# Optimization experiments

Hardware: AMD Instinct MI355X
Metric: run time of the kernel (lower is better)

Reference implementation:

```python
import jax, jax.numpy as jnp
import numpy as np

N_NODES = 40000
N_EDGES = 640000
D = 128
NEG_SLOPE = 0.2
EPS = 0.0  # init_eps=0, learn_eps=False -> constant buffer


def setup_inputs() -> dict:
    key = jax.random.key(0)
    ks = jax.random.split(key, 9)
    return {
        "feat": jax.random.normal(ks[0], (N_NODES, D), dtype=jnp.float32),
        "W_src": jax.random.normal(ks[1], (D, D), dtype=jnp.float32) * 0.1,
        "W_dst": jax.random.normal(ks[2], (D, D), dtype=jnp.float32) * 0.1,
        "W_src2": jax.random.normal(ks[3], (D, D), dtype=jnp.float32) * 0.1,
        "W_dst2": jax.random.normal(ks[4], (D, D), dtype=jnp.float32) * 0.1,
        "attn_l": jax.random.normal(ks[5], (D,), dtype=jnp.float32) * 0.1,
        "attn_r": jax.random.normal(ks[6], (D,), dtype=jnp.float32) * 0.1,
        "src": jax.random.randint(ks[7], (N_EDGES,), 0, N_NODES, dtype=jnp.int32),
        "dst": jax.random.randint(ks[8], (N_EDGES,), 0, N_NODES, dtype=jnp.int32),
    }


def reference(feat, W_src, W_dst, W_src2, W_dst2, attn_l, attn_r, src, dst):
    n = feat.shape[0]
    # Four linear projections (no bias), nn.Linear applies x @ W.T
    fs1 = feat @ W_src.T    # [N, D] -> messages for GIN sum
    fd1 = feat @ W_dst.T    # [N, D] -> self term
    fs2 = feat @ W_src2.T   # [N, D] -> attention-weighted messages
    fd2 = feat @ W_dst2.T   # [N, D]

    # GAT-style per-node attention logits
    el = jnp.sum(fs2 * attn_l, axis=-1)  # [N]
    er = jnp.sum(fd2 * attn_r, axis=-1)  # [N]

    # Per-edge score: u_add_v + leaky_relu
    e = el[src] + er[dst]                                   # [E]
    e = jnp.where(e >= 0, e, NEG_SLOPE * e)

    # edge_softmax: segment-wise softmax over edges grouped by dst
    seg_max = jax.ops.segment_max(e, dst, num_segments=n)   # [N]
    seg_max = jnp.where(jnp.isfinite(seg_max), seg_max, 0.0)
    ex = jnp.exp(e - seg_max[dst])                          # [E]
    denom = jax.ops.segment_sum(ex, dst, num_segments=n)    # [N]
    a = ex / denom[dst]                                     # [E]

    # update_all(copy_u, sum): plain neighbor sum of fs1
    neigh = jax.ops.segment_sum(fs1[src], dst, num_segments=n)            # [N, D]
    # update_all(u_mul_e, sum): attention-weighted sum of fs2
    add_ft = jax.ops.segment_sum(fs2[src] * a[:, None], dst, num_segments=n)  # [N, D]

    rst = (1.0 + EPS) * fd1 + neigh + add_ft
    return rst
```

## Files before the change

kernel.cpp:

```cpp
#include <hip/hip_runtime.h>
#include <math.h>

#define N_NODES 40000
#define N_EDGES 640000
#define D 128
#define NEG_SLOPE 0.2f
#define BCAP 64

typedef __bf16 bf16x8 __attribute__((ext_vector_type(8)));
typedef float f32x4 __attribute__((ext_vector_type(4)));

__device__ __forceinline__ unsigned short f2bf(float f) {
    unsigned int u = __float_as_uint(f);
    return (unsigned short)((u + 0x7fffu + ((u >> 16) & 1u)) >> 16);
}
__device__ __forceinline__ float bflo(unsigned int u) { return __uint_as_float(u << 16); }
__device__ __forceinline__ float bfhi(unsigned int u) { return __uint_as_float(u & 0xffff0000u); }

__global__ void k_zero_v(uint4* __restrict__ cnt4,
                         const float* __restrict__ Ws2, const float* __restrict__ Wd2,
                         const float* __restrict__ attn_l, const float* __restrict__ attn_r,
                         float* __restrict__ v_l, float* __restrict__ v_r) {
    if (blockIdx.x == 40) {
        int t = threadIdx.x;
        if (t < 128) {
            float s = 0.0f;
            for (int j = 0; j < D; ++j) s += attn_l[j] * Ws2[j * D + t];
            v_l[t] = s;
        } else {
            int k = t - 128;
            float s = 0.0f;
            for (int j = 0; j < D; ++j) s += attn_r[j] * Wd2[j * D + k];
            v_r[k] = s;
        }
        return;
    }
    int i = blockIdx.x * 256 + threadIdx.x;
    if (i < 10000) cnt4[i] = make_uint4(0, 0, 0, 0);
}

__global__ void k_setup(const float* __restrict__ Ws, const float* __restrict__ Ws2,
                        const float* __restrict__ Wd,
                        unsigned short* __restrict__ Wfrag,
                        const float* __restrict__ v_l, const float* __restrict__ v_r,
                        const int* __restrict__ src, const int* __restrict__ dst,
                        int* __restrict__ cnt, unsigned short* __restrict__ bucket,
                        const float* __restrict__ feat, unsigned int* __restrict__ featb,
                        float* __restrict__ el, float* __restrict__ er) {
    if (blockIdx.x < 625) {
        int t = blockIdx.x * 256 + threadIdx.x;
        #pragma unroll
        for (int j = 0; j < 4; ++j) {
            int e = t + j * 160000;
            int d = dst[e];
            int s = src[e];
            int slot = atomicAdd(&cnt[d], 1);
            if (slot < BCAP) bucket[(size_t)d * BCAP + slot] = (unsigned short)s;
        }
        return;
    }
    if (blockIdx.x < 817) {
        int idx = (blockIdx.x - 625) * 256 + threadIdx.x;
        int e    = idx & 7;
        int lane = (idx >> 3) & 63;
        int ks   = (idx >> 9) & 3;
        int ct   = (idx >> 11) & 7;
        int m    = idx >> 14;
        int col  = ct * 16 + (lane & 15);
        int k    = ks * 32 + (lane >> 4) * 8 + e;
        const float* W = (m == 0) ? Ws : (m == 1) ? Ws2 : Wd;
        Wfrag[idx] = f2bf(W[col * D + k]);
        return;
    }
    int idx = blockIdx.x - 817;
    int row = idx * 16 + (threadIdx.x >> 4);
    int c   = threadIdx.x & 15;
    const float* fp = feat + (size_t)row * D + c * 8;
    float4 p = *(const float4*)fp;
    float4 q = *(const float4*)(fp + 4);
    uint4 u;
    u.x = (unsigned int)f2bf(p.x) | ((unsigned int)f2bf(p.y) << 16);
    u.y = (unsigned int)f2bf(p.z) | ((unsigned int)f2bf(p.w) << 16);
    u.z = (unsigned int)f2bf(q.x) | ((unsigned int)f2bf(q.y) << 16);
    u.w = (unsigned int)f2bf(q.z) | ((unsigned int)f2bf(q.w) << 16);
    *(uint4*)(featb + (size_t)row * 64 + c * 4) = u;
    const float* vlp = v_l + c * 8;
    const float* vrp = v_r + c * 8;
    float4 l0 = *(const float4*)vlp, l1 = *(const float4*)(vlp + 4);
    float4 r0 = *(const float4*)vrp, r1 = *(const float4*)(vrp + 4);
    float sl = p.x*l0.x + p.y*l0.y + p.z*l0.z + p.w*l0.w
             + q.x*l1.x + q.y*l1.y + q.z*l1.z + q.w*l1.w;
    float sr = p.x*r0.x + p.y*r0.y + p.z*r0.z + p.w*r0.w
             + q.x*r1.x + q.y*r1.y + q.z*r1.z + q.w*r1.w;
    #pragma unroll
    for (int w = 1; w <= 8; w <<= 1) {
        sl += __shfl_xor(sl, w);
        sr += __shfl_xor(sr, w);
    }
    if (c == 0) { el[row] = sl; er[row] = sr; }
}

__global__ __launch_bounds__(256) void k_aggregate(
    const int* __restrict__ cnt, const unsigned short* __restrict__ bucket,
    const float* __restrict__ el, const float* __restrict__ er,
    const unsigned int* __restrict__ featb,
    unsigned int* __restrict__ agg1b, unsigned int* __restrict__ agg2b)
{
    const int node = blockIdx.x * 4 + (threadIdx.x >> 6);
    const int lane = threadIdx.x & 63;
    if (node >= N_NODES) return;
    int deg = cnt[node];
    deg = (deg > BCAP) ? BCAP : deg;

    const int q = lane & 15;
    const int g = lane >> 4;
    float A1[8], A2[8];
    #pragma unroll
    for (int c = 0; c < 8; ++c) { A1[c] = 0.f; A2[c] = 0.f; }

    if (deg > 0) {
        const int base = node * BCAP;
        int s_l = bucket[base + lane];
        if (lane >= deg) s_l = 0;

        uint4 v[8];
        #pragma unroll
        for (int j = 0; j < 8; ++j) {
            int eidx = (j >> 2) * 16 + (j & 3) * 4 + g;
            int s = __shfl(s_l, eidx);
            v[j] = *(const uint4*)(featb + (size_t)s * 64 + q * 4);
        }

        const float ern = er[node];
        float e = -INFINITY;
        if (lane < deg) {
            e = el[s_l] + ern;
            e = (e >= 0.f) ? e : NEG_SLOPE * e;
        }
        float mx = e;
        #pragma unroll
        for (int w = 32; w >= 1; w >>= 1) mx = fmaxf(mx, __shfl_xor(mx, w));
        float p = (lane < deg) ? __expf(e - mx) : 0.f;
        float ssum = p;
        #pragma unroll
        for (int w = 32; w >= 1; w >>= 1) ssum += __shfl_xor(ssum, w);
        float a_l = p / ssum;

        #pragma unroll
        for (int j = 0; j < 4; ++j) {
            int eidx = (j & 3) * 4 + g;
            float av = __shfl(a_l, eidx);
            float wf = (eidx < deg) ? 1.0f : 0.0f;
            float x0 = bflo(v[j].x), x1 = bfhi(v[j].x);
            float x2 = bflo(v[j].y), x3 = bfhi(v[j].y);
            float x4 = bflo(v[j].z), x5 = bfhi(v[j].z);
            float x6 = bflo(v[j].w), x7 = bfhi(v[j].w);
            A1[0] += wf * x0; A2[0] += av * x0;
            A1[1] += wf * x1; A2[1] += av * x1;
            A1[2] += wf * x2; A2[2] += av * x2;
            A1[3] += wf * x3; A2[3] += av * x3;
            A1[4] += wf * x4; A2[4] += av * x4;
            A1[5] += wf * x5; A2[5] += av * x5;
            A1[6] += wf * x6; A2[6] += av * x6;
            A1[7] += wf * x7; A2[7] += av * x7;
        }
        if (deg > 16) {
            #pragma unroll
            for (int j = 4; j < 8; ++j) {
                int eidx = 16 + (j & 3) * 4 + g;
                float av = __shfl(a_l, eidx);
                float wf = (eidx < deg) ? 1.0f : 0.0f;
                float x0 = bflo(v[j].x), x1 = bfhi(v[j].x);
                float x2 = bflo(v[j].y), x3 = bfhi(v[j].y);
                float x4 = bflo(v[j].z), x5 = bfhi(v[j].z);
                float x6 = bflo(v[j].w), x7 = bfhi(v[j].w);
                A1[0] += wf * x0; A2[0] += av * x0;
                A1[1] += wf * x1; A2[1] += av * x1;
                A1[2] += wf * x2; A2[2] += av * x2;
                A1[3] += wf * x3; A2[3] += av * x3;
                A1[4] += wf * x4; A2[4] += av * x4;
                A1[5] += wf * x5; A2[5] += av * x5;
                A1[6] += wf * x6; A2[6] += av * x6;
                A1[7] += wf * x7; A2[7] += av * x7;
            }
            for (int i = 32; i < deg; i += 16) {
                uint4 vt[4];
                float av[4], wf[4];
                #pragma unroll
                for (int j = 0; j < 4; ++j) {
                    int eidx = i + j * 4 + g;
                    int s = __shfl(s_l, eidx);
                    av[j] = __shfl(a_l, eidx);
                    wf[j] = (eidx < deg) ? 1.0f : 0.0f;
                    vt[j] = *(const uint4*)(featb + (size_t)s * 64 + q * 4);
                }
                #pragma unroll
                for (int j = 0; j < 4; ++j) {
                    float x0 = bflo(vt[j].x), x1 = bfhi(vt[j].x);
                    float x2 = bflo(vt[j].y), x3 = bfhi(vt[j].y);
                    float x4 = bflo(vt[j].z), x5 = bfhi(vt[j].z);
                    float x6 = bflo(vt[j].w), x7 = bfhi(vt[j].w);
                    A1[0] += wf[j] * x0; A2[0] += av[j] * x0;
                    A1[1] += wf[j] * x1; A2[1] += av[j] * x1;
                    A1[2] += wf[j] * x2; A2[2] += av[j] * x2;
                    A1[3] += wf[j] * x3; A2[3] += av[j] * x3;
                    A1[4] += wf[j] * x4; A2[4] += av[j] * x4;
                    A1[5] += wf[j] * x5; A2[5] += av[j] * x5;
                    A1[6] += wf[j] * x6; A2[6] += av[j] * x6;
                    A1[7] += wf[j] * x7; A2[7] += av[j] * x7;
                }
            }
        }

        #pragma unroll
        for (int c = 0; c < 8; ++c) {
            A1[c] += __shfl_xor(A1[c], 16); A1[c] += __shfl_xor(A1[c], 32);
            A2[c] += __shfl_xor(A2[c], 16); A2[c] += __shfl_xor(A2[c], 32);
        }
    }

    if (lane < 16) {
        uint4 u1, u2;
        u1.x = (unsigned int)f2bf(A1[0]) | ((unsigned int)f2bf(A1[1]) << 16);
        u1.y = (unsigned int)f2bf(A1[2]) | ((unsigned int)f2bf(A1[3]) << 16);
        u1.z = (unsigned int)f2bf(A1[4]) | ((unsigned int)f2bf(A1[5]) << 16);
        u1.w = (unsigned int)f2bf(A1[6]) | ((unsigned int)f2bf(A1[7]) << 16);
        u2.x = (unsigned int)f2bf(A2[0]) | ((unsigned int)f2bf(A2[1]) << 16);
        u2.y = (unsigned int)f2bf(A2[2]) | ((unsigned int)f2bf(A2[3]) << 16);
        u2.z = (unsigned int)f2bf(A2[4]) | ((unsigned int)f2bf(A2[5]) << 16);
        u2.w = (unsigned int)f2bf(A2[6]) | ((unsigned int)f2bf(A2[7]) << 16);
        *(uint4*)(agg1b + (size_t)node * 64 + q * 4) = u1;
        *(uint4*)(agg2b + (size_t)node * 64 + q * 4) = u2;
    }
}

__global__ __launch_bounds__(256) void k_gemm_all(
    const unsigned int* __restrict__ featb,
    const unsigned int* __restrict__ agg1b, const unsigned int* __restrict__ agg2b,
    const unsigned short* __restrict__ Wfrag, float* __restrict__ out)
{
    const int lane = threadIdx.x & 63;
    const int wave = threadIdx.x >> 6;
    const int tile = blockIdx.x >> 1;
    const int cth  = (blockIdx.x & 1) * 4;
    const int row0 = tile * 64 + wave * 16;
    const int arow = row0 + (lane & 15);
    const int koff = (lane >> 4) * 4;

    bf16x8 af[4], a1[4], a2[4];
    #pragma unroll
    for (int ks = 0; ks < 4; ++ks) {
        size_t o = (size_t)arow * 64 + ks * 16 + koff;
        af[ks] = *(const bf16x8*)(featb + o);
        a1[ks] = *(const bf16x8*)(agg1b + o);
        a2[ks] = *(const bf16x8*)(agg2b + o);
    }

    const bf16x8* wf0 = (const bf16x8*)Wfrag;
    const bf16x8* wf1 = wf0 + (size_t)(8 * 4) * 64;
    const bf16x8* wf2 = wf0 + (size_t)(2 * 8 * 4) * 64;

    f32x4 acc[4];
    #pragma unroll
    for (int c = 0; c < 4; ++c) acc[c] = (f32x4){0.f, 0.f, 0.f, 0.f};
    #pragma unroll
    for (int ks = 0; ks < 4; ++ks) {
        #pragma unroll
        for (int c = 0; c < 4; ++c) {
            const size_t bo = (size_t)((cth + c) * 4 + ks) * 64 + lane;
            acc[c] = __builtin_amdgcn_mfma_f32_16x16x32_bf16(af[ks], wf2[bo], acc[c], 0, 0, 0);
            acc[c] = __builtin_amdgcn_mfma_f32_16x16x32_bf16(a1[ks], wf0[bo], acc[c], 0, 0, 0);
            acc[c] = __builtin_amdgcn_mfma_f32_16x16x32_bf16(a2[ks], wf1[bo], acc[c], 0, 0, 0);
        }
    }

    const int rbase = row0 + (lane >> 4) * 4;
    const int cbase = lane & 15;
    #pragma unroll
    for (int c = 0; c < 4; ++c)
        #pragma unroll
        for (int r = 0; r < 4; ++r)
            out[(size_t)(rbase + r) * D + (cth + c) * 16 + cbase] = acc[c][r];
}

extern "C" void kernel_launch(void* const* d_in, const int* in_sizes, int n_in,
                              void* d_out, int out_size, void* d_ws, size_t ws_size,
                              hipStream_t stream) {
    const float* feat   = (const float*)d_in[0];
    const float* W_src  = (const float*)d_in[1];
    const float* W_dst  = (const float*)d_in[2];
    const float* W_src2 = (const float*)d_in[3];
    const float* W_dst2 = (const float*)d_in[4];
    const float* attn_l = (const float*)d_in[5];
    const float* attn_r = (const float*)d_in[6];
    const int*   src    = (const int*)d_in[7];
    const int*   dst    = (const int*)d_in[8];
    float* out = (float*)d_out;

    char* w = (char*)d_ws;
    float* v_l = (float*)w;                       w += 128 * 4;
    float* v_r = (float*)w;                       w += 128 * 4;
    float* el  = (float*)w;                       w += N_NODES * 4;
    float* er  = (float*)w;                       w += N_NODES * 4;
    int* cnt   = (int*)w;                         w += N_NODES * 4;
    unsigned int* featb = (unsigned int*)w;       w += (size_t)N_NODES * 64 * 4;
    unsigned int* agg1b = (unsigned int*)w;       w += (size_t)N_NODES * 64 * 4;
    unsigned int* agg2b = (unsigned int*)w;       w += (size_t)N_NODES * 64 * 4;
    unsigned short* bucket = (unsigned short*)w;  w += (size_t)N_NODES * BCAP * 2;
    unsigned short* Wfrag = (unsigned short*)w;   w += 3 * 8 * 4 * 64 * 8 * 2;

    k_zero_v<<<41, 256, 0, stream>>>((uint4*)cnt, W_src2, W_dst2, attn_l, attn_r, v_l, v_r);

    k_setup<<<3317, 256, 0, stream>>>(W_src, W_src2, W_dst, Wfrag, v_l, v_r,
                                      src, dst, cnt, bucket, feat, featb, el, er);

    k_aggregate<<<(N_NODES + 3) / 4, 256, 0, stream>>>(cnt, bucket, el, er,
                                                       featb, agg1b, agg2b);

    k_gemm_all<<<1250, 256, 0, stream>>>(featb, agg1b, agg2b, Wfrag, out);
}
```

Before: 98.73 us.

## Replace per-node global atomics with two-phase binned bucketing via shared-memory counters

```diff
diff --git a/kernel.cpp b/kernel.cpp
--- a/kernel.cpp
+++ b/kernel.cpp
@@ -6,6 +6,8 @@
 #define D 128
 #define NEG_SLOPE 0.2f
 #define BCAP 64
+#define NBINS 1250
+#define BINCAP 1024
 
 typedef __bf16 bf16x8 __attribute__((ext_vector_type(8)));
 typedef float f32x4 __attribute__((ext_vector_type(4)));
@@ -17,11 +19,11 @@
 __device__ __forceinline__ float bflo(unsigned int u) { return __uint_as_float(u << 16); }
 __device__ __forceinline__ float bfhi(unsigned int u) { return __uint_as_float(u & 0xffff0000u); }
 
-__global__ void k_zero_v(uint4* __restrict__ cnt4,
+__global__ void k_zero_v(int* __restrict__ binCnt,
                          const float* __restrict__ Ws2, const float* __restrict__ Wd2,
                          const float* __restrict__ attn_l, const float* __restrict__ attn_r,
                          float* __restrict__ v_l, float* __restrict__ v_r) {
-    if (blockIdx.x == 40) {
+    if (blockIdx.x == 5) {
         int t = threadIdx.x;
         if (t < 128) {
             float s = 0.0f;
@@ -36,7 +38,7 @@
         return;
     }
     int i = blockIdx.x * 256 + threadIdx.x;
-    if (i < 10000) cnt4[i] = make_uint4(0, 0, 0, 0);
+    if (i < NBINS) binCnt[i] = 0;
 }
 
 __global__ void k_setup(const float* __restrict__ Ws, const float* __restrict__ Ws2,
@@ -44,7 +46,7 @@
                         unsigned short* __restrict__ Wfrag,
                         const float* __restrict__ v_l, const float* __restrict__ v_r,
                         const int* __restrict__ src, const int* __restrict__ dst,
-                        int* __restrict__ cnt, unsigned short* __restrict__ bucket,
+                        int* __restrict__ binCnt, unsigned int* __restrict__ binBuf,
                         const float* __restrict__ feat, unsigned int* __restrict__ featb,
                         float* __restrict__ el, float* __restrict__ er) {
     if (blockIdx.x < 625) {
@@ -54,8 +56,11 @@
             int e = t + j * 160000;
             int d = dst[e];
             int s = src[e];
-            int slot = atomicAdd(&cnt[d], 1);
-            if (slot < BCAP) bucket[(size_t)d * BCAP + slot] = (unsigned short)s;
+            int b = d >> 5;
+            int dlow = d & 31;
+            int slot = atomicAdd(&binCnt[b], 1);
+            if (slot < BINCAP)
+                binBuf[(size_t)b * BINCAP + slot] = (unsigned int)s | ((unsigned int)dlow << 16);
         }
         return;
     }
@@ -100,6 +105,31 @@
     if (c == 0) { el[row] = sl; er[row] = sr; }
 }
 
+__global__ __launch_bounds__(256) void k_phaseB(
+    const int* __restrict__ binCnt, const unsigned int* __restrict__ binBuf,
+    unsigned short* __restrict__ bucket, int* __restrict__ cnt)
+{
+    __shared__ int lcnt[32];
+    const int b = blockIdx.x;
+    if (threadIdx.x < 32) lcnt[threadIdx.x] = 0;
+    __syncthreads();
+    int n = binCnt[b];
+    n = (n > BINCAP) ? BINCAP : n;
+    for (int i = threadIdx.x; i < n; i += 256) {
+        unsigned int ent = binBuf[(size_t)b * BINCAP + i];
+        int s    = ent & 0xffff;
+        int dlow = ent >> 16;
+        int slot = atomicAdd(&lcnt[dlow], 1);
+        if (slot < BCAP)
+            bucket[(size_t)(b * 32 + dlow) * BCAP + slot] = (unsigned short)s;
+    }
+    __syncthreads();
+    if (threadIdx.x < 32) {
+        int v = lcnt[threadIdx.x];
+        cnt[b * 32 + threadIdx.x] = (v > BCAP) ? BCAP : v;
+    }
+}
+
 __global__ __launch_bounds__(256) void k_aggregate(
     const int* __restrict__ cnt, const unsigned short* __restrict__ bucket,
     const float* __restrict__ el, const float* __restrict__ er,
@@ -110,7 +140,6 @@
     const int lane = threadIdx.x & 63;
     if (node >= N_NODES) return;
     int deg = cnt[node];
-    deg = (deg > BCAP) ? BCAP : deg;
 
     const int q = lane & 15;
     const int g = lane >> 4;
@@ -303,16 +332,20 @@
     float* el  = (float*)w;                       w += N_NODES * 4;
     float* er  = (float*)w;                       w += N_NODES * 4;
     int* cnt   = (int*)w;                         w += N_NODES * 4;
+    int* binCnt = (int*)w;                        w += 1280 * 4;
     unsigned int* featb = (unsigned int*)w;       w += (size_t)N_NODES * 64 * 4;
     unsigned int* agg1b = (unsigned int*)w;       w += (size_t)N_NODES * 64 * 4;
     unsigned int* agg2b = (unsigned int*)w;       w += (size_t)N_NODES * 64 * 4;
+    unsigned int* binBuf = (unsigned int*)w;      w += (size_t)NBINS * BINCAP * 4;
     unsigned short* bucket = (unsigned short*)w;  w += (size_t)N_NODES * BCAP * 2;
     unsigned short* Wfrag = (unsigned short*)w;   w += 3 * 8 * 4 * 64 * 8 * 2;
 
-    k_zero_v<<<41, 256, 0, stream>>>((uint4*)cnt, W_src2, W_dst2, attn_l, attn_r, v_l, v_r);
+    k_zero_v<<<6, 256, 0, stream>>>(binCnt, W_src2, W_dst2, attn_l, attn_r, v_l, v_r);
 
     k_setup<<<3317, 256, 0, stream>>>(W_src, W_src2, W_dst, Wfrag, v_l, v_r,
-                                      src, dst, cnt, bucket, feat, featb, el, er);
+                                      src, dst, binCnt, binBuf, feat, featb, el, er);
+
+    k_phaseB<<<NBINS, 256, 0, stream>>>(binCnt, binBuf, bucket, cnt);
 
     k_aggregate<<<(N_NODES + 3) / 4, 256, 0, stream>>>(cnt, bucket, el, er,
                                                        featb, agg1b, agg2b);
```

Measured after the change: 181.0 us. 1.83x slower.
